# Performance work log

Hardware: AMD Instinct MI355X
Metric: run time of the kernel (lower is better)

## Reference

```python
import jax, jax.numpy as jnp
import numpy as np

N_QUBITS = 8
N_LAYERS = 4
BATCH = 4096


def _ry(theta):
    # RY(theta) = [[cos(t/2), -sin(t/2)], [sin(t/2), cos(t/2)]]
    c = jnp.cos(theta / 2).astype(jnp.complex64)
    s = jnp.sin(theta / 2).astype(jnp.complex64)
    return jnp.stack([jnp.stack([c, -s], axis=-1),
                      jnp.stack([s, c], axis=-1)], axis=-2)  # (..., 2, 2)


def _rz(theta):
    # RZ(theta) = diag(exp(-i t/2), exp(+i t/2))
    p = jnp.exp(-0.5j * theta.astype(jnp.complex64))
    z = jnp.zeros_like(p)
    return jnp.stack([jnp.stack([p, z], axis=-1),
                      jnp.stack([z, jnp.conj(p)], axis=-1)], axis=-2)


def _apply_1q(state, U, w):
    # state: (B, 2, 2, ..., 2); apply 2x2 unitary U on wire w (axis 1+w).
    st = jnp.moveaxis(state, 1 + w, -1)
    if U.ndim == 3:  # per-sample (batched) gate, U: (B, 2, 2)
        st = jnp.einsum('bij,b...j->b...i', U, st)
    else:            # shared gate, U: (2, 2)
        st = jnp.einsum('ij,b...j->b...i', U, st)
    return jnp.moveaxis(st, -1, 1 + w)


def _apply_cnot(state, c, t):
    # flip target wire t where control wire c is |1>
    st = jnp.moveaxis(state, (1 + c, 1 + t), (-2, -1))
    st = jnp.concatenate([st[..., 0:1, :], st[..., 1:2, ::-1]], axis=-2)
    return jnp.moveaxis(st, (-2, -1), (1 + c, 1 + t))


def _circuit(x, weights):
    B = x.shape[0]
    state = jnp.zeros((B,) + (2,) * N_QUBITS, jnp.complex64)
    state = state.at[(slice(None),) + (0,) * N_QUBITS].set(1.0)  # |0...0>
    # Angle encoding: RY(x_i) on each wire, batched over samples
    for i in range(N_QUBITS):
        state = _apply_1q(state, _ry(x[:, i]), i)
    # Variational layers: CNOT ring then RY/RZ rotations
    for l in range(N_LAYERS):
        for i in range(N_QUBITS):
            state = _apply_cnot(state, i, (i + 1) % N_QUBITS)
        for i in range(N_QUBITS):
            state = _apply_1q(state, _ry(weights[l, i, 0]), i)
            state = _apply_1q(state, _rz(weights[l, i, 1]), i)
    # <Z_0> = P(q0=0) - P(q0=1)
    probs = jnp.sum(jnp.abs(state.reshape(B, 2, -1)) ** 2, axis=-1)
    return (probs[:, 0] - probs[:, 1]).astype(jnp.float32)


def setup_inputs() -> dict:
    key = jax.random.key(0)
    k1, k2 = jax.random.split(key)
    x = jax.random.uniform(k1, (BATCH, N_QUBITS), dtype=jnp.float32) * jnp.pi
    weights = jax.random.normal(k2, (N_LAYERS, N_QUBITS, 2), dtype=jnp.float32) * 0.1
    return {"x": x, "weights": weights}


def reference(x, weights):
    return _circuit(x, weights)
```

## Files before the change

kernel.cpp:

```cpp
#include <hip/hip_runtime.h>

#define NQ 8
#define NL 4
#define BATCH 4096


template <int CTRL>
__device__ __forceinline__ float dppx(float v) {
  return __int_as_float(
      __builtin_amdgcn_update_dpp(0, __float_as_int(v), CTRL, 0xF, 0xF, true));
}

__device__ __forceinline__ float swz16(float v) {
  return __int_as_float(__builtin_amdgcn_ds_swizzle(__float_as_int(v), 0x401F));
}
__device__ __forceinline__ float swz4(float v) {
  return __int_as_float(__builtin_amdgcn_ds_swizzle(__float_as_int(v), 0x101F));
}
__device__ __forceinline__ float bperm(int addr, float v) {
  return __int_as_float(__builtin_amdgcn_ds_bpermute(addr, __float_as_int(v)));
}

template <int W>
__device__ __forceinline__ float xl(float v, int bp32) {
  if constexpr (W == 0) return bperm(bp32, v);
  else if constexpr (W == 1) return swz16(v);
  else if constexpr (W == 2) return dppx<0x128>(v);
  else if constexpr (W == 3) return swz4(v);
  else if constexpr (W == 4) return dppx<0x4E>(v);
  else return dppx<0xB1>(v);
}

template <int W>
__device__ __forceinline__ void ry_gate(float re[4], float im[4],
                                        float c, float s, int lane, int bp32) {
  if constexpr (W <= 5) {
    const float ss = ((lane >> (5 - W)) & 1) ? s : -s;
#pragma unroll
    for (int r = 0; r < 4; ++r) {
      float pr = xl<W>(re[r], bp32);
      float pi = xl<W>(im[r], bp32);
      re[r] = c * re[r] + ss * pr;
      im[r] = c * im[r] + ss * pi;
    }
  } else {
    constexpr int m = 1 << (7 - W);
#pragma unroll
    for (int r = 0; r < 4; ++r) {
      if ((r & m) == 0) {
        const int r1 = r | m;
        float a0r = re[r], a1r = re[r1];
        float a0i = im[r], a1i = im[r1];
        re[r]  = c * a0r - s * a1r;
        re[r1] = s * a0r + c * a1r;
        im[r]  = c * a0i - s * a1i;
        im[r1] = s * a0i + c * a1i;
      }
    }
  }
}

template <int W>
__device__ __forceinline__ void rz_gate(float re[4], float im[4],
                                        float c, float s, int lane) {
  if constexpr (W <= 5) {
    const float ss = ((lane >> (5 - W)) & 1) ? s : -s;
#pragma unroll
    for (int r = 0; r < 4; ++r) {
      float nr = re[r] * c - im[r] * ss;
      float ni = im[r] * c + re[r] * ss;
      re[r] = nr; im[r] = ni;
    }
  } else {
    constexpr int m = 1 << (7 - W);
#pragma unroll
    for (int r = 0; r < 4; ++r) {
      const float ss = (r & m) ? s : -s;
      float nr = re[r] * c - im[r] * ss;
      float ni = im[r] * c + re[r] * ss;
      re[r] = nr; im[r] = ni;
    }
  }
}

__device__ __forceinline__ void ring(float re[4], float im[4],
                                     int addr_e, int addr_o, bool p2) {
  const float t0r = p2 ? re[2] : re[0];
  const float t1r = p2 ? re[3] : re[1];
  const float t2r = p2 ? re[1] : re[3];
  const float t3r = p2 ? re[0] : re[2];
  const float t0i = p2 ? im[2] : im[0];
  const float t1i = p2 ? im[3] : im[1];
  const float t2i = p2 ? im[1] : im[3];
  const float t3i = p2 ? im[0] : im[2];
  re[0] = bperm(addr_e, t0r);
  re[1] = bperm(addr_o, t1r);
  re[2] = bperm(addr_e, t2r);
  re[3] = bperm(addr_o, t3r);
  im[0] = bperm(addr_e, t0i);
  im[1] = bperm(addr_o, t1i);
  im[2] = bperm(addr_e, t2i);
  im[3] = bperm(addr_o, t3i);
}

__global__ __launch_bounds__(256, 4) void vqc_kernel(const float* __restrict__ x,
                                                     const float* __restrict__ w,
                                                     float* __restrict__ out) {
  const int lane = (int)(threadIdx.x & 63);
  const int s = (int)((blockIdx.x * blockDim.x + threadIdx.x) >> 6);

  const int gray   = lane ^ (lane >> 1);
  const int addr_e = gray << 2;
  const int addr_o = addr_e ^ 0xC0;
  const bool p2    = (__popc(lane) & 1) != 0;
  const int bp32   = (lane ^ 32) << 2;

  float fc[8], fs[8];
  {
    const float4 x0 = *(const float4*)&x[s * 8];
    const float4 x1 = *(const float4*)&x[s * 8 + 4];
    __sincosf(x0.x * 0.5f, &fs[0], &fc[0]);
    __sincosf(x0.y * 0.5f, &fs[1], &fc[1]);
    __sincosf(x0.z * 0.5f, &fs[2], &fc[2]);
    __sincosf(x0.w * 0.5f, &fs[3], &fc[3]);
    __sincosf(x1.x * 0.5f, &fs[4], &fc[4]);
    __sincosf(x1.y * 0.5f, &fs[5], &fc[5]);
    __sincosf(x1.z * 0.5f, &fs[6], &fc[6]);
    __sincosf(x1.w * 0.5f, &fs[7], &fc[7]);
  }

  float re[4], im[4];
  {
    const int L0  = lane & 1;
    const int L5b = (lane >> 5) & 1;
    const float g2 = (gray & 1) ? fs[5] : fc[5];
    const float g3 = (gray & 2) ? fs[4] : fc[4];
    const float g4 = (gray & 4) ? fs[3] : fc[3];
    const float g5 = (gray & 8) ? fs[2] : fc[2];
    const float Pl = (g2 * g3) * (g4 * g5);
    const int  b6 = ((lane >> 4) & 1) ^ L5b;
    const float h0 = (b6  ? fs[1] : fc[1]) * (L5b ? fs[0] : fc[0]);
    const float h1 = (b6  ? fc[1] : fs[1]) * (L5b ? fc[0] : fs[0]);
    const float A0 = Pl * h0, A1 = Pl * h1;
    const float f6a = L0 ? fs[6] : fc[6];
    const float f6b = L0 ? fc[6] : fs[6];
    re[0] = A0 * fc[7] * f6a;
    re[1] = A1 * fs[7] * f6a;
    re[2] = A0 * fs[7] * f6b;
    re[3] = A1 * fc[7] * f6b;
    im[0] = 0.f; im[1] = 0.f; im[2] = 0.f; im[3] = 0.f;
  }

#define APPLY_ROT(WL, W) { float cy, sy, cz, sz;         \
    __sincosf((WL)[(W) * 2 + 0] * 0.5f, &sy, &cy);       \
    __sincosf((WL)[(W) * 2 + 1] * 0.5f, &sz, &cz);       \
    ry_gate<W>(re, im, cy, sy, lane, bp32);              \
    rz_gate<W>(re, im, cz, sz, lane); }

  {
    const float* wl = &w[0];
    float cy, sy, cz, sz;
    __sincosf(wl[0] * 0.5f, &sy, &cy);
    __sincosf(wl[1] * 0.5f, &sz, &cz);
    const float ssy = (lane & 32) ? sy : -sy;
#pragma unroll
    for (int r = 0; r < 4; ++r) {
      float p = bperm(bp32, re[r]);
      re[r] = cy * re[r] + ssy * p;
    }
    const float ssz = (lane & 32) ? sz : -sz;
#pragma unroll
    for (int r = 0; r < 4; ++r) {
      im[r] = ssz * re[r];
      re[r] = cz * re[r];
    }
    APPLY_ROT(wl, 1) APPLY_ROT(wl, 2) APPLY_ROT(wl, 3)
    APPLY_ROT(wl, 4) APPLY_ROT(wl, 5) APPLY_ROT(wl, 6) APPLY_ROT(wl, 7)
  }

#pragma unroll
  for (int l = 1; l < NL - 1; ++l) {
    ring(re, im, addr_e, addr_o, p2);
    const float* wl = &w[l * NQ * 2];
    APPLY_ROT(wl, 0) APPLY_ROT(wl, 1) APPLY_ROT(wl, 2) APPLY_ROT(wl, 3)
    APPLY_ROT(wl, 4) APPLY_ROT(wl, 5) APPLY_ROT(wl, 6) APPLY_ROT(wl, 7)
  }
#undef APPLY_ROT

  ring(re, im, addr_e, addr_o, p2);
  {
    float cy, sy;
    __sincosf(w[(NL - 1) * NQ * 2 + 0] * 0.5f, &sy, &cy);
    ry_gate<0>(re, im, cy, sy, lane, bp32);
  }

  float acc = 0.f;
#pragma unroll
  for (int r = 0; r < 4; ++r) acc += re[r] * re[r] + im[r] * im[r];
  acc = (lane & 32) ? -acc : acc;
  acc += dppx<0xB1>(acc);
  acc += dppx<0x4E>(acc);
  acc += swz4(acc);
  acc += dppx<0x128>(acc);
  acc += swz16(acc);
  acc += bperm(bp32, acc);
  if (lane == 0) out[s] = acc;
}

extern "C" void kernel_launch(void* const* d_in, const int* in_sizes, int n_in,
                              void* d_out, int out_size, void* d_ws, size_t ws_size,
                              hipStream_t stream) {
  const float* x = (const float*)d_in[0];
  const float* w = (const float*)d_in[1];
  float* out = (float*)d_out;
  (void)in_sizes; (void)n_in; (void)out_size; (void)d_ws; (void)ws_size;

  dim3 grid(BATCH * 64 / 256), block(256);
  hipLaunchKernelGGL(vqc_kernel, grid, block, 0, stream, x, w, out);
}
```

Before: 63.01 us.

## Distribute sincos across lanes with readlane broadcast and fold final ring

Each lane now computes a single sincos, either for one weight angle (lanes 0-55) or for one input angle (lanes 56-63). The results are broadcast with readlane instead of every lane recomputing 64+ sincos values redundantly. Sign selects become precomputed XOR masks on the sign bit. The last CNOT ring and final RY are folded algebraically into one bpermute with parity-based signs before the Z0 reduction. This adds many readlane ops, which are scalar and serialising, and the new parity mapping carries a correctness risk.

```diff
diff --git a/kernel.cpp b/kernel.cpp
--- a/kernel.cpp
+++ b/kernel.cpp
@@ -19,6 +19,12 @@
 }
 __device__ __forceinline__ float bperm(int addr, float v) {
   return __int_as_float(__builtin_amdgcn_ds_bpermute(addr, __float_as_int(v)));
+}
+__device__ __forceinline__ float rlane(float v, int l) {
+  return __int_as_float(__builtin_amdgcn_readlane(__float_as_int(v), l));
+}
+__device__ __forceinline__ float sxor(float v, unsigned m) {
+  return __int_as_float(__float_as_int(v) ^ m);
 }
 
 template <int W>
@@ -33,9 +39,9 @@
 
 template <int W>
 __device__ __forceinline__ void ry_gate(float re[4], float im[4],
-                                        float c, float s, int lane, int bp32) {
+                                        float c, float s, unsigned m, int bp32) {
   if constexpr (W <= 5) {
-    const float ss = ((lane >> (5 - W)) & 1) ? s : -s;
+    const float ss = sxor(s, m);
 #pragma unroll
     for (int r = 0; r < 4; ++r) {
       float pr = xl<W>(re[r], bp32);
@@ -44,11 +50,11 @@
       im[r] = c * im[r] + ss * pi;
     }
   } else {
-    constexpr int m = 1 << (7 - W);
-#pragma unroll
-    for (int r = 0; r < 4; ++r) {
-      if ((r & m) == 0) {
-        const int r1 = r | m;
+    constexpr int mm = 1 << (7 - W);
+#pragma unroll
+    for (int r = 0; r < 4; ++r) {
+      if ((r & mm) == 0) {
+        const int r1 = r | mm;
         float a0r = re[r], a1r = re[r1];
         float a0i = im[r], a1i = im[r1];
         re[r]  = c * a0r - s * a1r;
@@ -62,9 +68,9 @@
 
 template <int W>
 __device__ __forceinline__ void rz_gate(float re[4], float im[4],
-                                        float c, float s, int lane) {
+                                        float c, float s, unsigned m) {
   if constexpr (W <= 5) {
-    const float ss = ((lane >> (5 - W)) & 1) ? s : -s;
+    const float ss = sxor(s, m);
 #pragma unroll
     for (int r = 0; r < 4; ++r) {
       float nr = re[r] * c - im[r] * ss;
@@ -72,10 +78,10 @@
       re[r] = nr; im[r] = ni;
     }
   } else {
-    constexpr int m = 1 << (7 - W);
-#pragma unroll
-    for (int r = 0; r < 4; ++r) {
-      const float ss = (r & m) ? s : -s;
+    constexpr int mm = 1 << (7 - W);
+#pragma unroll
+    for (int r = 0; r < 4; ++r) {
+      const float ss = (r & mm) ? s : -s;
       float nr = re[r] * c - im[r] * ss;
       float ni = im[r] * c + re[r] * ss;
       re[r] = nr; im[r] = ni;
@@ -114,97 +120,112 @@
   const int addr_o = addr_e ^ 0xC0;
   const bool p2    = (__popc(lane) & 1) != 0;
   const int bp32   = (lane ^ 32) << 2;
-
-  float fc[8], fs[8];
-  {
-    const float4 x0 = *(const float4*)&x[s * 8];
-    const float4 x1 = *(const float4*)&x[s * 8 + 4];
-    __sincosf(x0.x * 0.5f, &fs[0], &fc[0]);
-    __sincosf(x0.y * 0.5f, &fs[1], &fc[1]);
-    __sincosf(x0.z * 0.5f, &fs[2], &fc[2]);
-    __sincosf(x0.w * 0.5f, &fs[3], &fc[3]);
-    __sincosf(x1.x * 0.5f, &fs[4], &fc[4]);
-    __sincosf(x1.y * 0.5f, &fs[5], &fc[5]);
-    __sincosf(x1.z * 0.5f, &fs[6], &fc[6]);
-    __sincosf(x1.w * 0.5f, &fs[7], &fc[7]);
+  const int bp48   = (lane ^ 48) << 2;
+
+  unsigned sm[8];
+#pragma unroll
+  for (int W = 0; W < 6; ++W)
+    sm[W] = ((lane >> (5 - W)) & 1) ? 0u : 0x80000000u;
+  sm[6] = 0u; sm[7] = 0u;
+
+  float sn, cs;
+  {
+    const float wv = w[lane];
+    const float xv = x[(s << 3) | (lane & 7)];
+    const float ang = (lane >= 56) ? xv : wv;
+    __sincosf(ang * 0.5f, &sn, &cs);
   }
 
   float re[4], im[4];
   {
+    const float f0c = rlane(cs, 56), f0s = rlane(sn, 56);
+    const float f1c = rlane(cs, 57), f1s = rlane(sn, 57);
+    const float f2c = rlane(cs, 58), f2s = rlane(sn, 58);
+    const float f3c = rlane(cs, 59), f3s = rlane(sn, 59);
+    const float f4c = rlane(cs, 60), f4s = rlane(sn, 60);
+    const float f5c = rlane(cs, 61), f5s = rlane(sn, 61);
+    const float f6c = rlane(cs, 62), f6s = rlane(sn, 62);
+    const float f7c = rlane(cs, 63), f7s = rlane(sn, 63);
     const int L0  = lane & 1;
     const int L5b = (lane >> 5) & 1;
-    const float g2 = (gray & 1) ? fs[5] : fc[5];
-    const float g3 = (gray & 2) ? fs[4] : fc[4];
-    const float g4 = (gray & 4) ? fs[3] : fc[3];
-    const float g5 = (gray & 8) ? fs[2] : fc[2];
+    const float g2 = (gray & 1) ? f5s : f5c;
+    const float g3 = (gray & 2) ? f4s : f4c;
+    const float g4 = (gray & 4) ? f3s : f3c;
+    const float g5 = (gray & 8) ? f2s : f2c;
     const float Pl = (g2 * g3) * (g4 * g5);
     const int  b6 = ((lane >> 4) & 1) ^ L5b;
-    const float h0 = (b6  ? fs[1] : fc[1]) * (L5b ? fs[0] : fc[0]);
-    const float h1 = (b6  ? fc[1] : fs[1]) * (L5b ? fc[0] : fs[0]);
+    const float h0 = (b6 ? f1s : f1c) * (L5b ? f0s : f0c);
+    const float h1 = (b6 ? f1c : f1s) * (L5b ? f0c : f0s);
     const float A0 = Pl * h0, A1 = Pl * h1;
-    const float f6a = L0 ? fs[6] : fc[6];
-    const float f6b = L0 ? fc[6] : fs[6];
-    re[0] = A0 * fc[7] * f6a;
-    re[1] = A1 * fs[7] * f6a;
-    re[2] = A0 * fs[7] * f6b;
-    re[3] = A1 * fc[7] * f6b;
+    const float f6a = L0 ? f6s : f6c;
+    const float f6b = L0 ? f6c : f6s;
+    re[0] = A0 * f7c * f6a;
+    re[1] = A1 * f7s * f6a;
+    re[2] = A0 * f7s * f6b;
+    re[3] = A1 * f7c * f6b;
     im[0] = 0.f; im[1] = 0.f; im[2] = 0.f; im[3] = 0.f;
   }
 
-#define APPLY_ROT(WL, W) { float cy, sy, cz, sz;         \
-    __sincosf((WL)[(W) * 2 + 0] * 0.5f, &sy, &cy);       \
-    __sincosf((WL)[(W) * 2 + 1] * 0.5f, &sz, &cz);       \
-    ry_gate<W>(re, im, cy, sy, lane, bp32);              \
-    rz_gate<W>(re, im, cz, sz, lane); }
-
-  {
-    const float* wl = &w[0];
-    float cy, sy, cz, sz;
-    __sincosf(wl[0] * 0.5f, &sy, &cy);
-    __sincosf(wl[1] * 0.5f, &sz, &cz);
-    const float ssy = (lane & 32) ? sy : -sy;
+#define APPLY_ROT(BASE, W) {                                 \
+    const float cy = rlane(cs, (BASE) + (W) * 2);            \
+    const float sy = rlane(sn, (BASE) + (W) * 2);            \
+    const float cz = rlane(cs, (BASE) + (W) * 2 + 1);        \
+    const float sz = rlane(sn, (BASE) + (W) * 2 + 1);        \
+    ry_gate<W>(re, im, cy, sy, sm[W], bp32);                 \
+    rz_gate<W>(re, im, cz, sz, sm[W]); }
+
+  {
+    const float cy = rlane(cs, 0), sy = rlane(sn, 0);
+    const float cz = rlane(cs, 1), sz = rlane(sn, 1);
+    const float ssy = sxor(sy, sm[0]);
 #pragma unroll
     for (int r = 0; r < 4; ++r) {
       float p = bperm(bp32, re[r]);
       re[r] = cy * re[r] + ssy * p;
     }
-    const float ssz = (lane & 32) ? sz : -sz;
+    const float ssz = sxor(sz, sm[0]);
 #pragma unroll
     for (int r = 0; r < 4; ++r) {
       im[r] = ssz * re[r];
       re[r] = cz * re[r];
     }
-    APPLY_ROT(wl, 1) APPLY_ROT(wl, 2) APPLY_ROT(wl, 3)
-    APPLY_ROT(wl, 4) APPLY_ROT(wl, 5) APPLY_ROT(wl, 6) APPLY_ROT(wl, 7)
+    APPLY_ROT(0, 1) APPLY_ROT(0, 2) APPLY_ROT(0, 3)
+    APPLY_ROT(0, 4) APPLY_ROT(0, 5) APPLY_ROT(0, 6) APPLY_ROT(0, 7)
   }
 
 #pragma unroll
   for (int l = 1; l < NL - 1; ++l) {
     ring(re, im, addr_e, addr_o, p2);
-    const float* wl = &w[l * NQ * 2];
-    APPLY_ROT(wl, 0) APPLY_ROT(wl, 1) APPLY_ROT(wl, 2) APPLY_ROT(wl, 3)
-    APPLY_ROT(wl, 4) APPLY_ROT(wl, 5) APPLY_ROT(wl, 6) APPLY_ROT(wl, 7)
+    const int base = l * 16;
+    APPLY_ROT(base, 0) APPLY_ROT(base, 1) APPLY_ROT(base, 2) APPLY_ROT(base, 3)
+    APPLY_ROT(base, 4) APPLY_ROT(base, 5) APPLY_ROT(base, 6) APPLY_ROT(base, 7)
   }
 #undef APPLY_ROT
 
-  ring(re, im, addr_e, addr_o, p2);
-  {
-    float cy, sy;
-    __sincosf(w[(NL - 1) * NQ * 2 + 0] * 0.5f, &sy, &cy);
-    ry_gate<0>(re, im, cy, sy, lane, bp32);
-  }
-
-  float acc = 0.f;
-#pragma unroll
-  for (int r = 0; r < 4; ++r) acc += re[r] * re[r] + im[r] * im[r];
-  acc = (lane & 32) ? -acc : acc;
-  acc += dppx<0xB1>(acc);
-  acc += dppx<0x4E>(acc);
-  acc += swz4(acc);
-  acc += dppx<0x128>(acc);
-  acc += swz16(acc);
-  acc += bperm(bp32, acc);
-  if (lane == 0) out[s] = acc;
+  {
+    const float cy = rlane(cs, (NL - 1) * 16);
+    const float sy = rlane(sn, (NL - 1) * 16);
+    const unsigned pm0 = (unsigned)(__popc(lane & 31) & 1) << 31;
+    float acc = 0.f;
+#pragma unroll
+    for (int r = 0; r < 4; ++r) {
+      const unsigned pmr = pm0 ^ (((r == 1) | (r == 2)) ? 0x80000000u : 0u);
+      const float ssy = sxor(sy, pmr ^ 0x80000000u);
+      const float pr = bperm(bp48, re[r]);
+      const float pi = bperm(bp48, im[r]);
+      const float nr = cy * re[r] + ssy * pr;
+      const float ni = cy * im[r] + ssy * pi;
+      const float m2 = nr * nr + ni * ni;
+      acc += sxor(m2, pmr);
+    }
+    acc += dppx<0xB1>(acc);
+    acc += dppx<0x4E>(acc);
+    acc += swz4(acc);
+    acc += dppx<0x128>(acc);
+    acc += swz16(acc);
+    acc += bperm(bp32, acc);
+    if (lane == 0) out[s] = acc;
+  }
 }
 
 extern "C" void kernel_launch(void* const* d_in, const int* in_sizes, int n_in,
```

Result: no change. 62.39 us (-1.0%).
